# Kernel optimization log

Measured on AMD Instinct MI355X. Metric: run time of the kernel, lower is better.

## Reference

```python
import jax, jax.numpy as jnp
import numpy as np

N, E, D, H, G = 50000, 640000, 128, 128, 64
EPS = 1e-5


def gcn_conv(x, row, col, W, b, n):
    # PyG GCNConv: linear transform, symmetric deg^-1/2 normalization (self-loops
    # already appended to row/col), scatter-add aggregation, then bias.
    h = x @ W  # [N, H]
    ones = jnp.ones(row.shape[0], dtype=h.dtype)
    deg = jax.ops.segment_sum(ones, col, num_segments=n)
    dinv = jnp.where(deg > 0, jax.lax.rsqrt(deg), 0.0)
    norm = dinv[row] * dinv[col]                       # [E+N]
    msg = h[row] * norm[:, None]                       # gather + scale
    out = jax.ops.segment_sum(msg, col, num_segments=n)  # scatter-add
    return out + b


def graph_layernorm(x, w, b):
    # PyG LayerNorm(mode='graph') with batch=None: normalize over the whole tensor.
    mu = x.mean()
    xc = x - mu
    std = jnp.sqrt((xc * xc).mean())
    return xc / (std + EPS) * w + b


def setup_inputs() -> dict:
    key = jax.random.key(0)
    ks = jax.random.split(key, 12)
    x = jax.random.normal(ks[0], (N, D), dtype=jnp.float32)
    edge_index = jax.random.randint(ks[1], (2, E), 0, N, dtype=jnp.int64)
    batch = jnp.sort(jax.random.randint(ks[2], (N,), 0, G, dtype=jnp.int64))
    s1 = 1.0 / np.sqrt(D)
    s2 = 1.0 / np.sqrt(H)
    return {
        "x": x,
        "edge_index": edge_index,
        "batch": batch,
        "W1": jax.random.normal(ks[3], (D, H), dtype=jnp.float32) * s1,
        "b1": jnp.zeros((H,), dtype=jnp.float32),
        "ln1_w": jnp.ones((H,), dtype=jnp.float32),
        "ln1_b": jnp.zeros((H,), dtype=jnp.float32),
        "W2": jax.random.normal(ks[4], (H, H), dtype=jnp.float32) * s2,
        "b2": jnp.zeros((H,), dtype=jnp.float32),
        "ln2_w": jnp.ones((H,), dtype=jnp.float32),
        "ln2_b": jnp.zeros((H,), dtype=jnp.float32),
        "fc_w": jax.random.normal(ks[5], (H, 1), dtype=jnp.float32) * s2,
        "fc_b": jnp.zeros((1,), dtype=jnp.float32),
    }


def reference(x, edge_index, batch, W1, b1, ln1_w, ln1_b, W2, b2, ln2_w, ln2_b, fc_w, fc_b):
    n = x.shape[0]
    loops = jnp.arange(n, dtype=edge_index.dtype)
    row = jnp.concatenate([edge_index[0], loops])  # add self-loops
    col = jnp.concatenate([edge_index[1], loops])

    h = gcn_conv(x, row, col, W1, b1, n)
    h = jax.nn.relu(graph_layernorm(h, ln1_w, ln1_b))
    h = gcn_conv(h, row, col, W2, b2, n)
    h = jax.nn.relu(graph_layernorm(h, ln2_w, ln2_b))

    # global_mean_pool over batch segment ids
    sums = jax.ops.segment_sum(h, batch, num_segments=G)          # [G, H]
    cnt = jax.ops.segment_sum(jnp.ones((n,), h.dtype), batch, num_segments=G)
    pooled = sums / jnp.maximum(cnt, 1.0)[:, None]

    logits = pooled @ fc_w + fc_b                                  # [G, 1]
    return jax.nn.sigmoid(logits).squeeze(-1)                      # [G]
```

## Files before the change

kernel.cpp:

```cpp
#include <hip/hip_runtime.h>
#include <math.h>

#define H 128
#define PC 8

typedef _Float16 half8v __attribute__((ext_vector_type(8)));
typedef float floatx4 __attribute__((ext_vector_type(4)));

__device__ __forceinline__ int lower_bound_i(const int* a, int n, int key) {
  int lo = 0, hi = n;
  while (lo < hi) { int mid = (lo + hi) >> 1; if (a[mid] < key) lo = mid + 1; else hi = mid; }
  return lo;
}

__global__ void k_init(int* cntE, int* cursor, float* slots, int n) {
  int i = blockIdx.x * blockDim.x + threadIdx.x;
  int stride = gridDim.x * blockDim.x;
  for (int j = i; j < n; j += stride) { cntE[j] = 0; cursor[j] = 0; }
  for (int j = i; j < 256; j += stride) slots[j] = 0.f;
}

__global__ void k_count(const int* __restrict__ col, int* __restrict__ cntE, int E) {
  int e = blockIdx.x * blockDim.x + threadIdx.x;
  if (e < E) atomicAdd(&cntE[col[e]], 1);
}

__global__ void k_scan_block(const int* __restrict__ cnt, int* __restrict__ offs,
                             int* __restrict__ bsum, int n) {
  __shared__ int s[256];
  int tid = threadIdx.x;
  int i = blockIdx.x * 256 + tid;
  int v = (i < n) ? cnt[i] : 0;
  s[tid] = v;
  __syncthreads();
  for (int d = 1; d < 256; d <<= 1) {
    int t = (tid >= d) ? s[tid - d] : 0;
    __syncthreads();
    s[tid] += t;
    __syncthreads();
  }
  if (i < n) offs[i] = s[tid] - v;
  if (tid == 255) bsum[blockIdx.x] = s[255];
}

__global__ void k_scan_top(const int* __restrict__ bsum, int* __restrict__ boffs, int nb) {
  __shared__ int s[256];
  int tid = threadIdx.x;
  int v = (tid < nb) ? bsum[tid] : 0;
  s[tid] = v;
  __syncthreads();
  for (int d = 1; d < 256; d <<= 1) {
    int t = (tid >= d) ? s[tid - d] : 0;
    __syncthreads();
    s[tid] += t;
    __syncthreads();
  }
  boffs[tid] = s[tid] - v;
}

__global__ void k_scan_add(int* __restrict__ offs, const int* __restrict__ boffs,
                           const int* __restrict__ cntE, float* __restrict__ dinv, int n) {
  int i = blockIdx.x * 256 + threadIdx.x;
  if (i < n) {
    offs[i] += boffs[blockIdx.x];
    dinv[i] = rsqrtf((float)(cntE[i] + 1));
  }
}

__global__ void k_scatter(const int* __restrict__ row, const int* __restrict__ col,
                          const int* __restrict__ offs, int* __restrict__ cursor,
                          int* __restrict__ esrc, int E) {
  int e = blockIdx.x * blockDim.x + threadIdx.x;
  if (e < E) {
    int c = col[e];
    int p = atomicAdd(&cursor[c], 1);
    esrc[offs[c] + p] = row[e];
  }
}

__global__ void k_pack(const float* __restrict__ W1, const float* __restrict__ W2,
                       _Float16* __restrict__ PW1, _Float16* __restrict__ PW2) {
  int t = blockIdx.x * blockDim.x + threadIdx.x;
  const float* W = (t < 16384) ? W1 : W2;
  _Float16* PW = (t < 16384) ? PW1 : PW2;
  int u = t & 16383;
  int j = u & 7;
  int n = (u >> 3) & 15;
  int quad = (u >> 7) & 3;
  int ks = (u >> 9) & 3;
  int ct = (u >> 11) & 7;
  PW[u] = (_Float16)W[(ks * 32 + quad * 8 + j) * H + ct * 16 + n];
}

__global__ __launch_bounds__(256) void k_gemm_mfma(const float* __restrict__ Xf,
                                                   const _Float16* __restrict__ Xh,
                                                   const _Float16* __restrict__ PW,
                                                   _Float16* __restrict__ O,
                                                   const float* __restrict__ lnw,
                                                   const float* __restrict__ lnb,
                                                   const float* __restrict__ scal, int n) {
  int wave = blockIdx.x * 4 + (threadIdx.x >> 6);
  int tiles = (n + 15) >> 4;
  if (wave >= tiles) return;
  int lane = threadIdx.x & 63;
  int m = lane & 15;
  int quad = lane >> 4;
  int r0 = wave * 16;
  int row = r0 + m;
  if (row >= n) row = n - 1;

  bool ln = (scal != nullptr);
  float mu = ln ? scal[0] : 0.f;
  float rs = ln ? scal[1] : 0.f;

  floatx4 acc[8] = {};
  const half8v* PB8 = (const half8v*)PW;

#pragma unroll
  for (int ks = 0; ks < 4; ks++) {
    int kb = ks * 32 + quad * 8;
    half8v a;
    if (Xf) {
      const float* xr = Xf + (size_t)row * H + kb;
      float4 u0 = *(const float4*)xr;
      float4 u1 = *(const float4*)(xr + 4);
      a[0] = (_Float16)u0.x; a[1] = (_Float16)u0.y; a[2] = (_Float16)u0.z; a[3] = (_Float16)u0.w;
      a[4] = (_Float16)u1.x; a[5] = (_Float16)u1.y; a[6] = (_Float16)u1.z; a[7] = (_Float16)u1.w;
    } else {
      half8v hv = *(const half8v*)(Xh + (size_t)row * H + kb);
      if (ln) {
        float4 w0 = *(const float4*)(lnw + kb);
        float4 w1 = *(const float4*)(lnw + kb + 4);
        float4 c0 = *(const float4*)(lnb + kb);
        float4 c1 = *(const float4*)(lnb + kb + 4);
        a[0] = (_Float16)fmaxf(((float)hv[0] - mu) * rs * w0.x + c0.x, 0.f);
        a[1] = (_Float16)fmaxf(((float)hv[1] - mu) * rs * w0.y + c0.y, 0.f);
        a[2] = (_Float16)fmaxf(((float)hv[2] - mu) * rs * w0.z + c0.z, 0.f);
        a[3] = (_Float16)fmaxf(((float)hv[3] - mu) * rs * w0.w + c0.w, 0.f);
        a[4] = (_Float16)fmaxf(((float)hv[4] - mu) * rs * w1.x + c1.x, 0.f);
        a[5] = (_Float16)fmaxf(((float)hv[5] - mu) * rs * w1.y + c1.y, 0.f);
        a[6] = (_Float16)fmaxf(((float)hv[6] - mu) * rs * w1.z + c1.z, 0.f);
        a[7] = (_Float16)fmaxf(((float)hv[7] - mu) * rs * w1.w + c1.w, 0.f);
      } else {
        a = hv;
      }
    }
#pragma unroll
    for (int ct = 0; ct < 8; ct++) {
      half8v b = PB8[((ct * 4 + ks) * 4 + quad) * 16 + m];
      acc[ct] = __builtin_amdgcn_mfma_f32_16x16x32_f16(a, b, acc[ct], 0, 0, 0);
    }
  }

#pragma unroll
  for (int ct = 0; ct < 8; ct++) {
#pragma unroll
    for (int reg = 0; reg < 4; reg++) {
      int ro = r0 + quad * 4 + reg;
      if (ro < n) O[(size_t)ro * H + ct * 16 + m] = (_Float16)acc[ct][reg];
    }
  }
}

__global__ __launch_bounds__(256) void k_agg(const _Float16* __restrict__ Hs,
                                             _Float16* __restrict__ Out,
                                             const int* __restrict__ esrc, const int* __restrict__ offs,
                                             const int* __restrict__ cntE, const float* __restrict__ dinv,
                                             const float* __restrict__ bias, float* __restrict__ slot,
                                             int n) {
  int sub = threadIdx.x >> 4;
  int lane = threadIdx.x & 15;
  int i = blockIdx.x * 16 + sub;
  float sv = 0.f, sq = 0.f;
  if (i < n) {
    float di = dinv[i];
    half8v hself = *(const half8v*)&Hs[(size_t)i * H + 8 * lane];
    float acc[8];
#pragma unroll
    for (int e = 0; e < 8; e++) acc[e] = di * (float)hself[e];
    int beg = offs[i], cnt = cntE[i];
    for (int base = 0; base < cnt; base += 16) {
      int mm = cnt - base; if (mm > 16) mm = 16;
      int sid = 0; float dv = 0.f;
      if (lane < mm) { sid = esrc[beg + base + lane]; dv = dinv[sid]; }
      int j = 0;
      for (; j + 4 <= mm; j += 4) {
        int s0 = __shfl(sid, j + 0, 16);
        int s1 = __shfl(sid, j + 1, 16);
        int s2 = __shfl(sid, j + 2, 16);
        int s3 = __shfl(sid, j + 3, 16);
        float d0 = __shfl(dv, j + 0, 16);
        float d1 = __shfl(dv, j + 1, 16);
        float d2 = __shfl(dv, j + 2, 16);
        float d3 = __shfl(dv, j + 3, 16);
        half8v h0 = *(const half8v*)&Hs[(size_t)s0 * H + 8 * lane];
        half8v h1 = *(const half8v*)&Hs[(size_t)s1 * H + 8 * lane];
        half8v h2 = *(const half8v*)&Hs[(size_t)s2 * H + 8 * lane];
        half8v h3 = *(const half8v*)&Hs[(size_t)s3 * H + 8 * lane];
#pragma unroll
        for (int e = 0; e < 8; e++)
          acc[e] += d0 * (float)h0[e] + d1 * (float)h1[e] + d2 * (float)h2[e] + d3 * (float)h3[e];
      }
      for (; j < mm; j++) {
        int s = __shfl(sid, j, 16);
        float d = __shfl(dv, j, 16);
        half8v hv = *(const half8v*)&Hs[(size_t)s * H + 8 * lane];
#pragma unroll
        for (int e = 0; e < 8; e++) acc[e] += d * (float)hv[e];
      }
    }
    const float* bb = bias + 8 * lane;
    half8v vo;
#pragma unroll
    for (int e = 0; e < 8; e++) {
      float v = di * acc[e] + bb[e];
      vo[e] = (_Float16)v;
      sv += v;
      sq += v * v;
    }
    *(half8v*)&Out[(size_t)i * H + 8 * lane] = vo;
  }
#pragma unroll
  for (int o = 32; o > 0; o >>= 1) {
    sv += __shfl_xor(sv, o, 64);
    sq += __shfl_xor(sq, o, 64);
  }
  __shared__ float rsm[4], rqm[4];
  int wave = threadIdx.x >> 6;
  if ((threadIdx.x & 63) == 0) { rsm[wave] = sv; rqm[wave] = sq; }
  __syncthreads();
  if (threadIdx.x == 0) {
    float ts = rsm[0] + rsm[1] + rsm[2] + rsm[3];
    float tq = rqm[0] + rqm[1] + rqm[2] + rqm[3];
    int sl = blockIdx.x & 63;
    atomicAdd(&slot[sl], ts);
    atomicAdd(&slot[64 + sl], tq);
  }
}

__global__ void k_lnfin(const float* __restrict__ slot, float* __restrict__ scal, float invM) {
  int t = threadIdx.x;
  float s = slot[t], q = slot[64 + t];
#pragma unroll
  for (int o = 32; o > 0; o >>= 1) {
    s += __shfl_xor(s, o, 64);
    q += __shfl_xor(q, o, 64);
  }
  if (t == 0) {
    float mu = s * invM;
    float var = q * invM - mu * mu;
    var = fmaxf(var, 0.f);
    scal[0] = mu;
    scal[1] = 1.f / (sqrtf(var) + 1e-5f);
  }
}

__global__ __launch_bounds__(128) void k_pool(const _Float16* __restrict__ Hs, const int* __restrict__ batch,
                                              const float* __restrict__ lnw, const float* __restrict__ lnb,
                                              const float* __restrict__ scal, float* __restrict__ psum,
                                              int n) {
  int g = blockIdx.x / PC, q = blockIdx.x % PC;
  int t = threadIdx.x;
  int start = lower_bound_i(batch, n, g);
  int end = lower_bound_i(batch, n, g + 1);
  int tot = end - start;
  int per = (tot + PC - 1) / PC;
  int s = start + q * per;
  int e = s + per; if (e > end) e = end;
  float mu = scal[0], rs = scal[1];
  float w = lnw[t], bb = lnb[t];
  float acc = 0.f;
  for (int i = s; i < e; i++) {
    float v = (float)Hs[(size_t)i * H + t];
    v = (v - mu) * rs * w + bb;
    acc += fmaxf(v, 0.f);
  }
  psum[(size_t)blockIdx.x * H + t] = acc;
}

__global__ __launch_bounds__(128) void k_fc(const float* __restrict__ psum, const int* __restrict__ batch,
                                            const float* __restrict__ fcw, const float* __restrict__ fcb,
                                            float* __restrict__ out, int n) {
  int g = blockIdx.x;
  int t = threadIdx.x;
  int start = lower_bound_i(batch, n, g);
  int end = lower_bound_i(batch, n, g + 1);
  float cnt = fmaxf((float)(end - start), 1.f);
  float tot = 0.f;
#pragma unroll
  for (int c = 0; c < PC; c++) tot += psum[(size_t)(g * PC + c) * H + t];
  float v = tot / cnt * fcw[t];
  int lane = t & 63, wave = t >> 6;
#pragma unroll
  for (int o = 32; o > 0; o >>= 1) v += __shfl_xor(v, o, 64);
  __shared__ float r2[2];
  if (lane == 0) r2[wave] = v;
  __syncthreads();
  if (t == 0) {
    float logit = r2[0] + r2[1] + fcb[0];
    out[g] = 1.f / (1.f + expf(-logit));
  }
}

extern "C" void kernel_launch(void* const* d_in, const int* in_sizes, int n_in,
                              void* d_out, int out_size, void* d_ws, size_t ws_size,
                              hipStream_t stream) {
  const float* x    = (const float*)d_in[0];
  const int*   ei   = (const int*)d_in[1];
  const int*   batch= (const int*)d_in[2];
  const float* W1   = (const float*)d_in[3];
  const float* b1   = (const float*)d_in[4];
  const float* ln1w = (const float*)d_in[5];
  const float* ln1b = (const float*)d_in[6];
  const float* W2   = (const float*)d_in[7];
  const float* b2   = (const float*)d_in[8];
  const float* ln2w = (const float*)d_in[9];
  const float* ln2b = (const float*)d_in[10];
  const float* fcw  = (const float*)d_in[11];
  const float* fcb  = (const float*)d_in[12];
  float* out = (float*)d_out;

  int N = in_sizes[2];
  int E = in_sizes[1] / 2;
  int G = out_size;

  char* p = (char*)d_ws;
  int*   cntE   = (int*)p;   p += (size_t)N * 4;
  int*   offs   = (int*)p;   p += (size_t)N * 4;
  int*   cursor = (int*)p;   p += (size_t)N * 4;
  float* dinv   = (float*)p; p += (size_t)N * 4;
  int*   esrc   = (int*)p;   p += (size_t)E * 4;
  _Float16* bufA = (_Float16*)p; p += (size_t)N * H * 2;
  _Float16* bufB = (_Float16*)p; p += (size_t)N * H * 2;
  _Float16* PW1  = (_Float16*)p; p += 16384 * 2;
  _Float16* PW2  = (_Float16*)p; p += 16384 * 2;
  float* slots  = (float*)p; p += 256 * 4;
  float* scal   = (float*)p; p += 4 * 4;
  int*   bsum   = (int*)p;   p += 256 * 4;
  int*   boffs  = (int*)p;   p += 256 * 4;
  float* psum   = (float*)p; p += (size_t)G * PC * H * 4;

  const int* row = ei;
  const int* col = ei + E;

  k_init<<<256, 256, 0, stream>>>(cntE, cursor, slots, N);
  k_pack<<<128, 256, 0, stream>>>(W1, W2, PW1, PW2);
  k_count<<<(E + 255) / 256, 256, 0, stream>>>(col, cntE, E);
  int NB = (N + 255) / 256;
  k_scan_block<<<NB, 256, 0, stream>>>(cntE, offs, bsum, N);
  k_scan_top<<<1, 256, 0, stream>>>(bsum, boffs, NB);
  k_scan_add<<<NB, 256, 0, stream>>>(offs, boffs, cntE, dinv, N);
  k_scatter<<<(E + 255) / 256, 256, 0, stream>>>(row, col, offs, cursor, esrc, E);

  int tiles = (N + 15) / 16;
  int GB = (tiles + 3) / 4;
  float invM = 1.f / ((float)N * (float)H);

  k_gemm_mfma<<<GB, 256, 0, stream>>>(x, nullptr, PW1, bufA, nullptr, nullptr, nullptr, N);
  k_agg<<<(N + 15) / 16, 256, 0, stream>>>(bufA, bufB, esrc, offs, cntE, dinv, b1, slots, N);
  k_lnfin<<<1, 64, 0, stream>>>(slots, scal, invM);
  k_gemm_mfma<<<GB, 256, 0, stream>>>(nullptr, bufB, PW2, bufA, ln1w, ln1b, scal, N);
  k_agg<<<(N + 15) / 16, 256, 0, stream>>>(bufA, bufB, esrc, offs, cntE, dinv, b2, slots + 128, N);
  k_lnfin<<<1, 64, 0, stream>>>(slots + 128, scal + 2, invM);
  k_pool<<<G * PC, 128, 0, stream>>>(bufB, batch, ln2w, ln2b, scal + 2, psum, N);
  k_fc<<<G, 128, 0, stream>>>(psum, batch, fcw, fcb, out, N);
}
```

Baseline: 300.9 us.

## Merge small kernels and widen aggregation gather unroll to eight

Combines the init and weight-pack kernels into one launch and drops the top-level scan kernel: each scan-add block now sums the preceding block totals itself. The LayerNorm finalize kernels are removed, and the consumers (GEMM and pool) recompute mean and inverse std from the partial slots. The aggregation loop gains an 8-wide gather unroll so more row loads are in flight per step. This cuts four launches and their serialization gaps, at the cost of redundant per-block reductions and higher register pressure in the aggregation kernel.

New measurement: 299.1 us. About the same (-0.6%).

```diff
diff --git a/kernel.cpp b/kernel.cpp
--- a/kernel.cpp
+++ b/kernel.cpp
@@ -13,11 +13,28 @@
   return lo;
 }
 
-__global__ void k_init(int* cntE, int* cursor, float* slots, int n) {
-  int i = blockIdx.x * blockDim.x + threadIdx.x;
-  int stride = gridDim.x * blockDim.x;
-  for (int j = i; j < n; j += stride) { cntE[j] = 0; cursor[j] = 0; }
-  for (int j = i; j < 256; j += stride) slots[j] = 0.f;
+__global__ void k_initpack(const float* __restrict__ W1, const float* __restrict__ W2,
+                           _Float16* __restrict__ PW1, _Float16* __restrict__ PW2,
+                           int* cntE, int* cursor, float* slots, int n) {
+  int b = blockIdx.x;
+  int tid = threadIdx.x;
+  if (b < 128) {
+    int t = b * 256 + tid;
+    const float* W = (t < 16384) ? W1 : W2;
+    _Float16* PW = (t < 16384) ? PW1 : PW2;
+    int u = t & 16383;
+    int j = u & 7;
+    int nn = (u >> 3) & 15;
+    int quad = (u >> 7) & 3;
+    int ks = (u >> 9) & 3;
+    int ct = (u >> 11) & 7;
+    PW[u] = (_Float16)W[(ks * 32 + quad * 8 + j) * H + ct * 16 + nn];
+  } else {
+    int i = (b - 128) * 256 + tid;
+    int stride = 128 * 256;
+    for (int j = i; j < n; j += stride) { cntE[j] = 0; cursor[j] = 0; }
+    for (int j = i; j < 256; j += stride) slots[j] = 0.f;
+  }
 }
 
 __global__ void k_count(const int* __restrict__ col, int* __restrict__ cntE, int E) {
@@ -43,26 +60,19 @@
   if (tid == 255) bsum[blockIdx.x] = s[255];
 }
 
-__global__ void k_scan_top(const int* __restrict__ bsum, int* __restrict__ boffs, int nb) {
-  __shared__ int s[256];
+__global__ void k_scan_add(int* __restrict__ offs, const int* __restrict__ bsum,
+                           const int* __restrict__ cntE, float* __restrict__ dinv, int n) {
+  __shared__ int sh[4];
   int tid = threadIdx.x;
-  int v = (tid < nb) ? bsum[tid] : 0;
-  s[tid] = v;
+  int v = (tid < blockIdx.x) ? bsum[tid] : 0;
+#pragma unroll
+  for (int o = 32; o > 0; o >>= 1) v += __shfl_xor(v, o, 64);
+  if ((tid & 63) == 0) sh[tid >> 6] = v;
   __syncthreads();
-  for (int d = 1; d < 256; d <<= 1) {
-    int t = (tid >= d) ? s[tid - d] : 0;
-    __syncthreads();
-    s[tid] += t;
-    __syncthreads();
-  }
-  boffs[tid] = s[tid] - v;
-}
-
-__global__ void k_scan_add(int* __restrict__ offs, const int* __restrict__ boffs,
-                           const int* __restrict__ cntE, float* __restrict__ dinv, int n) {
-  int i = blockIdx.x * 256 + threadIdx.x;
+  int boff = sh[0] + sh[1] + sh[2] + sh[3];
+  int i = blockIdx.x * 256 + tid;
   if (i < n) {
-    offs[i] += boffs[blockIdx.x];
+    offs[i] += boff;
     dinv[i] = rsqrtf((float)(cntE[i] + 1));
   }
 }
@@ -78,27 +88,14 @@
   }
 }
 
-__global__ void k_pack(const float* __restrict__ W1, const float* __restrict__ W2,
-                       _Float16* __restrict__ PW1, _Float16* __restrict__ PW2) {
-  int t = blockIdx.x * blockDim.x + threadIdx.x;
-  const float* W = (t < 16384) ? W1 : W2;
-  _Float16* PW = (t < 16384) ? PW1 : PW2;
-  int u = t & 16383;
-  int j = u & 7;
-  int n = (u >> 3) & 15;
-  int quad = (u >> 7) & 3;
-  int ks = (u >> 9) & 3;
-  int ct = (u >> 11) & 7;
-  PW[u] = (_Float16)W[(ks * 32 + quad * 8 + j) * H + ct * 16 + n];
-}
-
 __global__ __launch_bounds__(256) void k_gemm_mfma(const float* __restrict__ Xf,
                                                    const _Float16* __restrict__ Xh,
                                                    const _Float16* __restrict__ PW,
                                                    _Float16* __restrict__ O,
                                                    const float* __restrict__ lnw,
                                                    const float* __restrict__ lnb,
-                                                   const float* __restrict__ scal, int n) {
+                                                   const float* __restrict__ slot,
+                                                   float invM, int n) {
   int wave = blockIdx.x * 4 + (threadIdx.x >> 6);
   int tiles = (n + 15) >> 4;
   if (wave >= tiles) return;
@@ -109,9 +106,16 @@
   int row = r0 + m;
   if (row >= n) row = n - 1;
 
-  bool ln = (scal != nullptr);
-  float mu = ln ? scal[0] : 0.f;
-  float rs = ln ? scal[1] : 0.f;
+  bool ln = (slot != nullptr);
+  float mu = 0.f, rs = 0.f;
+  if (ln) {
+    float s = slot[lane], q = slot[64 + lane];
+#pragma unroll
+    for (int o = 32; o > 0; o >>= 1) { s += __shfl_xor(s, o, 64); q += __shfl_xor(q, o, 64); }
+    mu = s * invM;
+    float var = fmaxf(q * invM - mu * mu, 0.f);
+    rs = 1.f / (sqrtf(var) + 1e-5f);
+  }
 
   floatx4 acc[8] = {};
   const half8v* PB8 = (const half8v*)PW;
@@ -184,6 +188,23 @@
       int sid = 0; float dv = 0.f;
       if (lane < mm) { sid = esrc[beg + base + lane]; dv = dinv[sid]; }
       int j = 0;
+      for (; j + 8 <= mm; j += 8) {
+        int sg[8]; float dg[8]; half8v hg[8];
+#pragma unroll
+        for (int u = 0; u < 8; u++) {
+          sg[u] = __shfl(sid, j + u, 16);
+          dg[u] = __shfl(dv, j + u, 16);
+        }
+#pragma unroll
+        for (int u = 0; u < 8; u++) hg[u] = *(const half8v*)&Hs[(size_t)sg[u] * H + 8 * lane];
+#pragma unroll
+        for (int e = 0; e < 8; e++) {
+          float t = 0.f;
+#pragma unroll
+          for (int u = 0; u < 8; u++) t += dg[u] * (float)hg[u][e];
+          acc[e] += t;
+        }
+      }
       for (; j + 4 <= mm; j += 4) {
         int s0 = __shfl(sid, j + 0, 16);
         int s1 = __shfl(sid, j + 1, 16);
@@ -238,39 +259,30 @@
   }
 }
 
-__global__ void k_lnfin(const float* __restrict__ slot, float* __restrict__ scal, float invM) {
-  int t = threadIdx.x;
-  float s = slot[t], q = slot[64 + t];
-#pragma unroll
-  for (int o = 32; o > 0; o >>= 1) {
-    s += __shfl_xor(s, o, 64);
-    q += __shfl_xor(q, o, 64);
-  }
-  if (t == 0) {
-    float mu = s * invM;
-    float var = q * invM - mu * mu;
-    var = fmaxf(var, 0.f);
-    scal[0] = mu;
-    scal[1] = 1.f / (sqrtf(var) + 1e-5f);
-  }
-}
-
-__global__ __launch_bounds__(128) void k_pool(const _Float16* __restrict__ Hs, const int* __restrict__ batch,
+__global__ __launch_bounds__(128) void k_pool(const _Float16* __restrict__ Hs,
+                                              const int* __restrict__ batch,
                                               const float* __restrict__ lnw, const float* __restrict__ lnb,
-                                              const float* __restrict__ scal, float* __restrict__ psum,
-                                              int n) {
+                                              const float* __restrict__ slot, float invM,
+                                              float* __restrict__ psum, int n) {
   int g = blockIdx.x / PC, q = blockIdx.x % PC;
   int t = threadIdx.x;
+  int l = t & 63;
+  float s = slot[l], qq = slot[64 + l];
+#pragma unroll
+  for (int o = 32; o > 0; o >>= 1) { s += __shfl_xor(s, o, 64); qq += __shfl_xor(qq, o, 64); }
+  float mu = s * invM;
+  float var = fmaxf(qq * invM - mu * mu, 0.f);
+  float rs = 1.f / (sqrtf(var) + 1e-5f);
+
   int start = lower_bound_i(batch, n, g);
   int end = lower_bound_i(batch, n, g + 1);
   int tot = end - start;
   int per = (tot + PC - 1) / PC;
-  int s = start + q * per;
-  int e = s + per; if (e > end) e = end;
-  float mu = scal[0], rs = scal[1];
+  int s0 = start + q * per;
+  int e0 = s0 + per; if (e0 > end) e0 = end;
   float w = lnw[t], bb = lnb[t];
   float acc = 0.f;
-  for (int i = s; i < e; i++) {
+  for (int i = s0; i < e0; i++) {
     float v = (float)Hs[(size_t)i * H + t];
     v = (v - mu) * rs * w + bb;
     acc += fmaxf(v, 0.f);
@@ -335,33 +347,27 @@
   _Float16* PW1  = (_Float16*)p; p += 16384 * 2;
   _Float16* PW2  = (_Float16*)p; p += 16384 * 2;
   float* slots  = (float*)p; p += 256 * 4;
-  float* scal   = (float*)p; p += 4 * 4;
   int*   bsum   = (int*)p;   p += 256 * 4;
-  int*   boffs  = (int*)p;   p += 256 * 4;
   float* psum   = (float*)p; p += (size_t)G * PC * H * 4;
 
   const int* row = ei;
   const int* col = ei + E;
 
-  k_init<<<256, 256, 0, stream>>>(cntE, cursor, slots, N);
-  k_pack<<<128, 256, 0, stream>>>(W1, W2, PW1, PW2);
+  k_initpack<<<256, 256, 0, stream>>>(W1, W2, PW1, PW2, cntE, cursor, slots, N);
   k_count<<<(E + 255) / 256, 256, 0, stream>>>(col, cntE, E);
   int NB = (N + 255) / 256;
   k_scan_block<<<NB, 256, 0, stream>>>(cntE, offs, bsum, N);
-  k_scan_top<<<1, 256, 0, stream>>>(bsum, boffs, NB);
-  k_scan_add<<<NB, 256, 0, stream>>>(offs, boffs, cntE, dinv, N);
+  k_scan_add<<<NB, 256, 0, stream>>>(offs, bsum, cntE, dinv, N);
   k_scatter<<<(E + 255) / 256, 256, 0, stream>>>(row, col, offs, cursor, esrc, E);
 
   int tiles = (N + 15) / 16;
   int GB = (tiles + 3) / 4;
   float invM = 1.f / ((float)N * (float)H);
 
-  k_gemm_mfma<<<GB, 256, 0, stream>>>(x, nullptr, PW1, bufA, nullptr, nullptr, nullptr, N);
+  k_gemm_mfma<<<GB, 256, 0, stream>>>(x, nullptr, PW1, bufA, nullptr, nullptr, nullptr, 0.f, N);
   k_agg<<<(N + 15) / 16, 256, 0, stream>>>(bufA, bufB, esrc, offs, cntE, dinv, b1, slots, N);
-  k_lnfin<<<1, 64, 0, stream>>>(slots, scal, invM);
-  k_gemm_mfma<<<GB, 256, 0, stream>>>(nullptr, bufB, PW2, bufA, ln1w, ln1b, scal, N);
+  k_gemm_mfma<<<GB, 256, 0, stream>>>(nullptr, bufB, PW2, bufA, ln1w, ln1b, slots, invM, N);
   k_agg<<<(N + 15) / 16, 256, 0, stream>>>(bufA, bufB, esrc, offs, cntE, dinv, b2, slots + 128, N);
-  k_lnfin<<<1, 64, 0, stream>>>(slots + 128, scal + 2, invM);
-  k_pool<<<G * PC, 128, 0, stream>>>(bufB, batch, ln2w, ln2b, scal + 2, psum, N);
+  k_pool<<<G * PC, 128, 0, stream>>>(bufB, batch, ln2w, ln2b, slots + 128, invM, psum, N);
   k_fc<<<G, 128, 0, stream>>>(psum, batch, fcw, fcb, out, N);
 }
```
